# Optimization experiments

Hardware: AMD Instinct MI355X
Metric: run time of the kernel (lower is better)

Reference implementation:

```python
import jax, jax.numpy as jnp
import numpy as np

B, C, H, W = 32, 512, 32, 32
TXT_DIM, M, NUM_HEADS = 768, 77, 8
HEAD_DIM = C // NUM_HEADS
SCALE = HEAD_DIM ** -0.5


def setup_inputs() -> dict:
    key = jax.random.key(0)
    ks = jax.random.split(key, 9)
    x = jax.random.normal(ks[0], (B, C, H, W), dtype=jnp.float32)
    text_emb = jax.random.normal(ks[1], (B, M, TXT_DIM), dtype=jnp.float32)
    attention_mask = jnp.ones((B, M), dtype=jnp.int32)
    # Linear params (PyTorch convention: weight [out, in], bias [out])
    s_q = 1.0 / np.sqrt(C)
    s_kv = 1.0 / np.sqrt(TXT_DIM)
    Wq = jax.random.uniform(ks[2], (C, C), jnp.float32, -s_q, s_q)
    bq = jax.random.uniform(ks[3], (C,), jnp.float32, -s_q, s_q)
    Wk = jax.random.uniform(ks[4], (C, TXT_DIM), jnp.float32, -s_kv, s_kv)
    bk = jax.random.uniform(ks[5], (C,), jnp.float32, -s_kv, s_kv)
    Wv = jax.random.uniform(ks[6], (C, TXT_DIM), jnp.float32, -s_kv, s_kv)
    bv = jax.random.uniform(ks[7], (C,), jnp.float32, -s_kv, s_kv)
    return {"x": x, "text_emb": text_emb, "attention_mask": attention_mask,
            "Wq": Wq, "bq": bq, "Wk": Wk, "bk": bk, "Wv": Wv, "bv": bv}


def reference(x, text_emb, attention_mask, Wq, bq, Wk, bk, Wv, bv):
    b, c, h, w = x.shape
    n = h * w
    x_flat = x.reshape(b, c, n).transpose(0, 2, 1)          # [B, N, C]
    Q = x_flat @ Wq.T + bq                                   # [B, N, C]
    K = text_emb @ Wk.T + bk                                 # [B, M, C]
    V = text_emb @ Wv.T + bv                                 # [B, M, C]
    Q = Q.reshape(b, n, NUM_HEADS, HEAD_DIM)
    K = K.reshape(b, -1, NUM_HEADS, HEAD_DIM)
    V = V.reshape(b, -1, NUM_HEADS, HEAD_DIM)
    # scores: [B, heads, N, M]
    scores = jnp.einsum('bnhd,bmhd->bhnm', Q, K) * SCALE
    mask = attention_mask[:, None, None, :] != 0
    scores = jnp.where(mask, scores, -jnp.inf)
    probs = jax.nn.softmax(scores, axis=-1)
    out = jnp.einsum('bhnm,bmhd->bnhd', probs, V)            # [B, N, heads, d]
    out = out.reshape(b, n, c).transpose(0, 2, 1).reshape(b, c, h, w)
    return out
```

## Files before the change

kernel.cpp:

```cpp
#include <hip/hip_runtime.h>
#include <math.h>

#define BB   32
#define CC   512
#define HWN  1024
#define MM   77
#define TXT  768
#define NH   8
#define HD   64
#define SCALEF 0.125f
#define MPAD 96
#define KVROWS (BB*MPAD)
#define AP   40
#define PP   104
#define OSP  132

typedef __attribute__((ext_vector_type(8))) short          bf16x8;
typedef __attribute__((ext_vector_type(8))) unsigned short us8;
typedef __attribute__((ext_vector_type(4))) float          f32x4;

__device__ inline unsigned short f2bf(float f) {
    union { float f; unsigned u; } v; v.f = f;
    unsigned r = v.u + 0x7fff + ((v.u >> 16) & 1);
    return (unsigned short)(r >> 16);
}

__device__ inline void gload_lds16(const void* g, void* l) {
    __builtin_amdgcn_global_load_lds(
        (const __attribute__((address_space(1))) void*)g,
        (__attribute__((address_space(3))) void*)l, 16, 0, 0);
}

__global__ __launch_bounds__(256) void wcvt_kernel(
    const float* __restrict__ src, unsigned short* __restrict__ dst)
{
    const int i = blockIdx.x * 256 + threadIdx.x;
    const float4 v = ((const float4*)src)[i];
    ushort4 o;
    o.x = f2bf(v.x); o.y = f2bf(v.y); o.z = f2bf(v.z); o.w = f2bf(v.w);
    ((ushort4*)dst)[i] = o;
}

__global__ __launch_bounds__(256) void tcvt_kernel(
    const float* __restrict__ x, unsigned short* __restrict__ xT)
{
    const int nt = blockIdx.x, ct = blockIdx.y, b = blockIdx.z;
    const int n0 = nt * 64, c0 = ct * 64;
    __shared__ float tile[64][65];
    const int t = threadIdx.x;
    const float* xb = x + (size_t)b * CC * HWN;
    {
        const int c = t >> 2;
        #pragma unroll
        for (int j = 0; j < 4; ++j) {
            const int f4 = (t & 3) + j * 4;
            const float4 v = *(const float4*)&xb[(size_t)(c0 + c) * HWN + n0 + f4 * 4];
            tile[c][f4 * 4 + 0] = v.x; tile[c][f4 * 4 + 1] = v.y;
            tile[c][f4 * 4 + 2] = v.z; tile[c][f4 * 4 + 3] = v.w;
        }
    }
    __syncthreads();
    unsigned short* xTb = xT + (size_t)b * HWN * CC;
    #pragma unroll
    for (int j = 0; j < 2; ++j) {
        const int n = (t >> 3) + j * 32;
        const int c8 = (t & 7) * 8;
        us8 o;
        #pragma unroll
        for (int i = 0; i < 8; ++i) o[i] = f2bf(tile[c8 + i][n]);
        *(us8*)&xTb[(size_t)(n0 + n) * CC + c0 + c8] = o;
    }
}

__global__ __launch_bounds__(256) void qgemm_mfma(
    const unsigned short* __restrict__ xT, const unsigned short* __restrict__ Wqb,
    const float* __restrict__ bq, unsigned short* __restrict__ Qb)
{
    const int rt = blockIdx.x, ct = blockIdx.y;
    const int row0 = rt * 128, co0 = ct * 128;
    __shared__ unsigned short As[128 * 32];
    __shared__ unsigned short Bs[128 * 32];
    const int t = threadIdx.x;
    const int lane = t & 63, w = t >> 6;
    const int wr = w >> 1, wc = w & 1;
    const int lm = lane & 15, quad = lane >> 4;
    const int lrow = lane >> 2, lk = (lane & 3) * 8;

    f32x4 acc[4][4] = {};

    for (int k0 = 0; k0 < CC; k0 += 32) {
        #pragma unroll
        for (int p = 0; p < 2; ++p) {
            const int chunk = w * 2 + p;
            gload_lds16(&xT[(size_t)(row0 + chunk * 16 + lrow) * CC + k0 + lk],
                        &As[chunk * 512]);
            gload_lds16(&Wqb[(size_t)(co0 + chunk * 16 + lrow) * CC + k0 + lk],
                        &Bs[chunk * 512]);
        }
        __syncthreads();
        bf16x8 a[4], bfr[4];
        #pragma unroll
        for (int i = 0; i < 4; ++i)
            a[i] = *(const bf16x8*)&As[(wr * 64 + i * 16 + lm) * 32 + quad * 8];
        #pragma unroll
        for (int i = 0; i < 4; ++i)
            bfr[i] = *(const bf16x8*)&Bs[(wc * 64 + i * 16 + lm) * 32 + quad * 8];
        #pragma unroll
        for (int mi = 0; mi < 4; ++mi)
            #pragma unroll
            for (int ni = 0; ni < 4; ++ni)
                acc[mi][ni] = __builtin_amdgcn_mfma_f32_16x16x32_bf16(
                    a[mi], bfr[ni], acc[mi][ni], 0, 0, 0);
        __syncthreads();
    }

    #pragma unroll
    for (int ni = 0; ni < 4; ++ni) {
        const int col = co0 + wc * 64 + ni * 16 + lm;
        const float bias = bq[col];
        #pragma unroll
        for (int mi = 0; mi < 4; ++mi) {
            #pragma unroll
            for (int j = 0; j < 4; ++j) {
                const int row = row0 + wr * 64 + mi * 16 + quad * 4 + j;
                Qb[(size_t)row * CC + col] = f2bf(acc[mi][ni][j] + bias);
            }
        }
    }
}

__global__ __launch_bounds__(256) void kvgemm_mfma(
    const float* __restrict__ te,
    const float* __restrict__ Wk, const float* __restrict__ bk,
    const float* __restrict__ Wv, const float* __restrict__ bv,
    unsigned short* __restrict__ Kb, unsigned short* __restrict__ Vt)
{
    const int rt = blockIdx.x, ctc = blockIdx.y;
    const int row0 = rt * 64;
    const int isV = (ctc >= 8);
    const float* W = isV ? Wv : Wk;
    const float* bias_p = isV ? bv : bk;
    const int co0 = (ctc & 7) * 64;

    __shared__ unsigned short As[64 * AP];
    __shared__ unsigned short Bs[64 * AP];
    const int t = threadIdx.x;
    const int lane = t & 63, w = t >> 6;
    const int wr = w >> 1, wc = w & 1;
    const int lm = lane & 15, quad = lane >> 4;
    const int chunk = t & 3, srow = t >> 2;

    f32x4 acc[2][2] = {};

    const int rflat = row0 + srow;
    const int b_i = rflat / MPAD, m_i = rflat % MPAD;
    const float* terow = te + ((size_t)b_i * MM + min(m_i, MM - 1)) * TXT;
    const float* wrow  = W + (size_t)(co0 + srow) * TXT;

    for (int k0 = 0; k0 < TXT; k0 += 32) {
        {
            const float4 f0 = *(const float4*)&terow[k0 + chunk * 8];
            const float4 f1 = *(const float4*)&terow[k0 + chunk * 8 + 4];
            us8 o;
            o[0] = f2bf(f0.x); o[1] = f2bf(f0.y); o[2] = f2bf(f0.z); o[3] = f2bf(f0.w);
            o[4] = f2bf(f1.x); o[5] = f2bf(f1.y); o[6] = f2bf(f1.z); o[7] = f2bf(f1.w);
            *(us8*)&As[srow * AP + chunk * 8] = o;

            const float4 g0 = *(const float4*)&wrow[k0 + chunk * 8];
            const float4 g1 = *(const float4*)&wrow[k0 + chunk * 8 + 4];
            us8 ob;
            ob[0] = f2bf(g0.x); ob[1] = f2bf(g0.y); ob[2] = f2bf(g0.z); ob[3] = f2bf(g0.w);
            ob[4] = f2bf(g1.x); ob[5] = f2bf(g1.y); ob[6] = f2bf(g1.z); ob[7] = f2bf(g1.w);
            *(us8*)&Bs[srow * AP + chunk * 8] = ob;
        }
        __syncthreads();
        bf16x8 a[2], bfr[2];
        #pragma unroll
        for (int i = 0; i < 2; ++i)
            a[i] = *(const bf16x8*)&As[(wr * 32 + i * 16 + lm) * AP + quad * 8];
        #pragma unroll
        for (int i = 0; i < 2; ++i)
            bfr[i] = *(const bf16x8*)&Bs[(wc * 32 + i * 16 + lm) * AP + quad * 8];
        #pragma unroll
        for (int mi = 0; mi < 2; ++mi)
            #pragma unroll
            for (int ni = 0; ni < 2; ++ni)
                acc[mi][ni] = __builtin_amdgcn_mfma_f32_16x16x32_bf16(
                    a[mi], bfr[ni], acc[mi][ni], 0, 0, 0);
        __syncthreads();
    }

    #pragma unroll
    for (int ni = 0; ni < 2; ++ni) {
        const int col = co0 + wc * 32 + ni * 16 + lm;
        const float bias = bias_p[col];
        #pragma unroll
        for (int mi = 0; mi < 2; ++mi) {
            #pragma unroll
            for (int j = 0; j < 2 * 2; ++j) {
                const int row = row0 + wr * 32 + mi * 16 + quad * 4 + j;
                const int bo = row / MPAD, mo = row % MPAD;
                const unsigned short hv = f2bf(acc[mi][ni][j] + bias);
                if (isV) {
                    Vt[((size_t)bo * CC + col) * MPAD + mo] = hv;
                } else if (mo < MM) {
                    Kb[((size_t)bo * MM + mo) * CC + col] = hv;
                }
            }
        }
    }
}

__global__ __launch_bounds__(256) void attn_mfma(
    const unsigned short* __restrict__ Qb, const unsigned short* __restrict__ Kb,
    const unsigned short* __restrict__ Vt, const int* __restrict__ amask,
    float* __restrict__ out)
{
    const int ntile = blockIdx.x;
    const int h     = blockIdx.y;
    const int b     = blockIdx.z;
    const int row0  = ntile * 128;

    __shared__ char smem[64 * OSP * 4];
    __shared__ float msk[80];
    unsigned short* Ps = (unsigned short*)smem;
    float* Os = (float*)smem;

    const int t = threadIdx.x;
    const int w = t >> 6, lane = t & 63;
    const int lm = lane & 15, quad = lane >> 4;

    {
        const int r = t >> 1, off = 80 + (t & 1) * 8;
        us8 z = {0, 0, 0, 0, 0, 0, 0, 0};
        *(us8*)&Ps[r * PP + off] = z;
    }
    if (t < 80) msk[t] = (t < MM && amask[b * MM + t] != 0) ? 0.f : -INFINITY;
    __syncthreads();

    f32x4 s[2][5] = {};
    const unsigned short* qbase = Qb + ((size_t)b * HWN + row0) * CC + h * HD;
    const unsigned short* kbase = Kb + (size_t)b * MM * CC + h * HD;
    #pragma unroll
    for (int ks = 0; ks < 2; ++ks) {
        bf16x8 a[2], kf[5];
        #pragma unroll
        for (int mt = 0; mt < 2; ++mt)
            a[mt] = *(const bf16x8*)&qbase[(size_t)((w * 2 + mt) * 16 + lm) * CC + ks * 32 + quad * 8];
        #pragma unroll
        for (int n = 0; n < 5; ++n) {
            const int kr = min(n * 16 + lm, MM - 1);
            kf[n] = *(const bf16x8*)&kbase[(size_t)kr * CC + ks * 32 + quad * 8];
        }
        #pragma unroll
        for (int mt = 0; mt < 2; ++mt)
            #pragma unroll
            for (int n = 0; n < 5; ++n)
                s[mt][n] = __builtin_amdgcn_mfma_f32_16x16x32_bf16(a[mt], kf[n], s[mt][n], 0, 0, 0);
    }

    float inv[2][4];
    #pragma unroll
    for (int mt = 0; mt < 2; ++mt) {
        #pragma unroll
        for (int j = 0; j < 4; ++j) {
            float v[5];
            #pragma unroll
            for (int n = 0; n < 5; ++n)
                v[n] = s[mt][n][j] * SCALEF + msk[n * 16 + lm];
            float mx = fmaxf(fmaxf(fmaxf(v[0], v[1]), fmaxf(v[2], v[3])), v[4]);
            mx = fmaxf(mx, __shfl_xor(mx, 1, 64));
            mx = fmaxf(mx, __shfl_xor(mx, 2, 64));
            mx = fmaxf(mx, __shfl_xor(mx, 4, 64));
            mx = fmaxf(mx, __shfl_xor(mx, 8, 64));
            float sum = 0.f;
            #pragma unroll
            for (int n = 0; n < 5; ++n) { v[n] = __expf(v[n] - mx); sum += v[n]; }
            sum += __shfl_xor(sum, 1, 64);
            sum += __shfl_xor(sum, 2, 64);
            sum += __shfl_xor(sum, 4, 64);
            sum += __shfl_xor(sum, 8, 64);
            inv[mt][j] = 1.0f / sum;
            const int mrow = (w * 2 + mt) * 16 + quad * 4 + j;
            #pragma unroll
            for (int n = 0; n < 5; ++n)
                Ps[mrow * PP + n * 16 + lm] = f2bf(v[n]);
        }
    }
    __syncthreads();

    f32x4 o[2][4] = {};
    const unsigned short* vbase = Vt + ((size_t)b * CC + h * HD) * MPAD;
    #pragma unroll
    for (int ks = 0; ks < 3; ++ks) {
        bf16x8 a[2], vf[4];
        #pragma unroll
        for (int mt = 0; mt < 2; ++mt)
            a[mt] = *(const bf16x8*)&Ps[((w * 2 + mt) * 16 + lm) * PP + ks * 32 + quad * 8];
        #pragma unroll
        for (int n = 0; n < 4; ++n)
            vf[n] = *(const bf16x8*)&vbase[(size_t)(n * 16 + lm) * MPAD + ks * 32 + quad * 8];
        #pragma unroll
        for (int mt = 0; mt < 2; ++mt)
            #pragma unroll
            for (int n = 0; n < 4; ++n)
                o[mt][n] = __builtin_amdgcn_mfma_f32_16x16x32_bf16(a[mt], vf[n], o[mt][n], 0, 0, 0);
    }
    __syncthreads();

    #pragma unroll
    for (int mt = 0; mt < 2; ++mt) {
        #pragma unroll
        for (int n = 0; n < 4; ++n) {
            const int col = n * 16 + lm;
            const int r0 = (w * 2 + mt) * 16 + quad * 4;
            float4 st;
            st.x = o[mt][n][0] * inv[mt][0];
            st.y = o[mt][n][1] * inv[mt][1];
            st.z = o[mt][n][2] * inv[mt][2];
            st.w = o[mt][n][3] * inv[mt][3];
            *(float4*)&Os[col * OSP + r0] = st;
        }
    }
    __syncthreads();

    float* obase = out + ((size_t)b * CC + h * HD) * HWN + row0;
    #pragma unroll
    for (int p = 0; p < 8; ++p) {
        const int idx = p * 256 + t;
        const int col = idx >> 5;
        const int r4  = idx & 31;
        const float4 v = *(const float4*)&Os[col * OSP + r4 * 4];
        *(float4*)&obase[(size_t)col * HWN + r4 * 4] = v;
    }
}

extern "C" void kernel_launch(void* const* d_in, const int* in_sizes, int n_in,
                              void* d_out, int out_size, void* d_ws, size_t ws_size,
                              hipStream_t stream)
{
    const float* x     = (const float*)d_in[0];
    const float* te    = (const float*)d_in[1];
    const int*   amask = (const int*)d_in[2];
    const float* Wq    = (const float*)d_in[3];
    const float* bq    = (const float*)d_in[4];
    const float* Wk    = (const float*)d_in[5];
    const float* bk    = (const float*)d_in[6];
    const float* Wv    = (const float*)d_in[7];
    const float* bv    = (const float*)d_in[8];
    float* out = (float*)d_out;

    unsigned short* xT  = (unsigned short*)d_ws;
    unsigned short* Qb  = xT + (size_t)BB * HWN * CC;
    unsigned short* Kb  = Qb + (size_t)BB * HWN * CC;
    unsigned short* Vt  = Kb + (size_t)BB * MM * CC;
    unsigned short* Wqb = Vt + (size_t)BB * CC * MPAD;

    wcvt_kernel<<<dim3(CC * CC / 4 / 256), 256, 0, stream>>>(Wq, Wqb);
    tcvt_kernel<<<dim3(16, 8, BB), 256, 0, stream>>>(x, xT);
    qgemm_mfma<<<dim3(256, 4), 256, 0, stream>>>(xT, Wqb, bq, Qb);
    kvgemm_mfma<<<dim3(KVROWS / 64, 16), 256, 0, stream>>>(te, Wk, bk, Wv, bv, Kb, Vt);
    attn_mfma<<<dim3(8, NH, BB), 256, 0, stream>>>(Qb, Kb, Vt, amask, out);
}
```

Baseline: 233.2 us.

## Merge conversion kernels and fuse Q/K/V GEMMs into one launch

Combines the weight conversion and the x transpose-convert into a single prep kernel that also pre-converts Wk, Wv and text_emb to bf16. The Q GEMM and the K/V GEMM become one kernel with a shared 128x128 tile path that loads directly into LDS, replacing the old K/V kernel's small 64x64 tiles with in-loop fp32->bf16 conversion. This cuts launches from five to three and lets the K/V work overlap with the Q GEMM tail, at the cost of extra workspace and a divergent prologue/epilogue.

```diff
diff --git a/kernel.cpp b/kernel.cpp
--- a/kernel.cpp
+++ b/kernel.cpp
@@ -11,7 +11,6 @@
 #define SCALEF 0.125f
 #define MPAD 96
 #define KVROWS (BB*MPAD)
-#define AP   40
 #define PP   104
 #define OSP  132
 
@@ -31,53 +30,73 @@
         (__attribute__((address_space(3))) void*)l, 16, 0, 0);
 }
 
-__global__ __launch_bounds__(256) void wcvt_kernel(
-    const float* __restrict__ src, unsigned short* __restrict__ dst)
+#define TGRID 4096
+#define CV_WQ 65536
+#define CV_WK 98304
+#define CV_WV 98304
+#define CV_TE 473088
+#define CVTOT (CV_WQ + CV_WK + CV_WV + CV_TE)
+
+__global__ __launch_bounds__(256) void prep_kernel(
+    const float* __restrict__ x, const float* __restrict__ te,
+    const float* __restrict__ Wq, const float* __restrict__ Wk,
+    const float* __restrict__ Wv,
+    unsigned short* __restrict__ xT, unsigned short* __restrict__ teb,
+    unsigned short* __restrict__ Wqb, unsigned short* __restrict__ Wkb,
+    unsigned short* __restrict__ Wvb)
 {
-    const int i = blockIdx.x * 256 + threadIdx.x;
-    const float4 v = ((const float4*)src)[i];
-    ushort4 o;
-    o.x = f2bf(v.x); o.y = f2bf(v.y); o.z = f2bf(v.z); o.w = f2bf(v.w);
-    ((ushort4*)dst)[i] = o;
-}
-
-__global__ __launch_bounds__(256) void tcvt_kernel(
-    const float* __restrict__ x, unsigned short* __restrict__ xT)
+    const int bid = blockIdx.x;
+    const int t = threadIdx.x;
+
+    if (bid < TGRID) {
+        const int nt = bid & 15, ct = (bid >> 4) & 7, b = bid >> 7;
+        const int n0 = nt * 64, c0 = ct * 64;
+        __shared__ float tile[64][65];
+        const float* xb = x + (size_t)b * CC * HWN;
+        {
+            const int c = t >> 2;
+            #pragma unroll
+            for (int j = 0; j < 4; ++j) {
+                const int f4 = (t & 3) + j * 4;
+                const float4 v = *(const float4*)&xb[(size_t)(c0 + c) * HWN + n0 + f4 * 4];
+                tile[c][f4 * 4 + 0] = v.x; tile[c][f4 * 4 + 1] = v.y;
+                tile[c][f4 * 4 + 2] = v.z; tile[c][f4 * 4 + 3] = v.w;
+            }
+        }
+        __syncthreads();
+        unsigned short* xTb = xT + (size_t)b * HWN * CC;
+        #pragma unroll
+        for (int j = 0; j < 2; ++j) {
+            const int n = (t >> 3) + j * 32;
+            const int c8 = (t & 7) * 8;
+            us8 o;
+            #pragma unroll
+            for (int i = 0; i < 8; ++i) o[i] = f2bf(tile[c8 + i][n]);
+            *(us8*)&xTb[(size_t)(n0 + n) * CC + c0 + c8] = o;
+        }
+    } else {
+        const int idx = (bid - TGRID) * 256 + t;
+        const float* src; unsigned short* dst; int off;
+        if (idx < CV_WQ)                    { src = Wq; dst = Wqb; off = idx; }
+        else if (idx < CV_WQ + CV_WK)       { src = Wk; dst = Wkb; off = idx - CV_WQ; }
+        else if (idx < CV_WQ + CV_WK + CV_WV) { src = Wv; dst = Wvb; off = idx - CV_WQ - CV_WK; }
+        else                                { src = te; dst = teb; off = idx - CV_WQ - CV_WK - CV_WV; }
+        const float4 v = ((const float4*)src)[off];
+        ushort4 o;
+        o.x = f2bf(v.x); o.y = f2bf(v.y); o.z = f2bf(v.z); o.w = f2bf(v.w);
+        ((ushort4*)dst)[off] = o;
+    }
+}
+
+__global__ __launch_bounds__(256) void gemm_all(
+    const unsigned short* __restrict__ xT, const unsigned short* __restrict__ Wqb,
+    const float* __restrict__ bq, unsigned short* __restrict__ Qb,
+    const unsigned short* __restrict__ teb,
+    const unsigned short* __restrict__ Wkb, const float* __restrict__ bk,
+    const unsigned short* __restrict__ Wvb, const float* __restrict__ bv,
+    unsigned short* __restrict__ Kb, unsigned short* __restrict__ Vt)
 {
-    const int nt = blockIdx.x, ct = blockIdx.y, b = blockIdx.z;
-    const int n0 = nt * 64, c0 = ct * 64;
-    __shared__ float tile[64][65];
-    const int t = threadIdx.x;
-    const float* xb = x + (size_t)b * CC * HWN;
-    {
-        const int c = t >> 2;
-        #pragma unroll
-        for (int j = 0; j < 4; ++j) {
-            const int f4 = (t & 3) + j * 4;
-            const float4 v = *(const float4*)&xb[(size_t)(c0 + c) * HWN + n0 + f4 * 4];
-            tile[c][f4 * 4 + 0] = v.x; tile[c][f4 * 4 + 1] = v.y;
-            tile[c][f4 * 4 + 2] = v.z; tile[c][f4 * 4 + 3] = v.w;
-        }
-    }
-    __syncthreads();
-    unsigned short* xTb = xT + (size_t)b * HWN * CC;
-    #pragma unroll
-    for (int j = 0; j < 2; ++j) {
-        const int n = (t >> 3) + j * 32;
-        const int c8 = (t & 7) * 8;
-        us8 o;
-        #pragma unroll
-        for (int i = 0; i < 8; ++i) o[i] = f2bf(tile[c8 + i][n]);
-        *(us8*)&xTb[(size_t)(n0 + n) * CC + c0 + c8] = o;
-    }
-}
-
-__global__ __launch_bounds__(256) void qgemm_mfma(
-    const unsigned short* __restrict__ xT, const unsigned short* __restrict__ Wqb,
-    const float* __restrict__ bq, unsigned short* __restrict__ Qb)
-{
-    const int rt = blockIdx.x, ct = blockIdx.y;
-    const int row0 = rt * 128, co0 = ct * 128;
+    const int bid = blockIdx.x;
     __shared__ unsigned short As[128 * 32];
     __shared__ unsigned short Bs[128 * 32];
     const int t = threadIdx.x;
@@ -86,17 +105,43 @@
     const int lm = lane & 15, quad = lane >> 4;
     const int lrow = lane >> 2, lk = (lane & 3) * 8;
 
+    const unsigned short *gA0, *gA1, *gB0, *gB1;
+    int kIters, mode, row0, co0;
+
+    if (bid < 1024) {
+        mode = 0;
+        const int rt = bid & 255, ct = bid >> 8;
+        row0 = rt * 128; co0 = ct * 128;
+        kIters = CC / 32;
+        gA0 = xT  + (size_t)(row0 + (w * 2 + 0) * 16 + lrow) * CC + lk;
+        gA1 = xT  + (size_t)(row0 + (w * 2 + 1) * 16 + lrow) * CC + lk;
+        gB0 = Wqb + (size_t)(co0 + (w * 2 + 0) * 16 + lrow) * CC + lk;
+        gB1 = Wqb + (size_t)(co0 + (w * 2 + 1) * 16 + lrow) * CC + lk;
+    } else {
+        const int id = bid - 1024;
+        const int rt = id % 24, cc = id / 24;
+        const int isV = (cc >= 4);
+        mode = isV ? 2 : 1;
+        row0 = rt * 128; co0 = (cc & 3) * 128;
+        kIters = TXT / 32;
+        const unsigned short* Wb = isV ? Wvb : Wkb;
+        const int rp0 = row0 + (w * 2 + 0) * 16 + lrow;
+        const int rp1 = row0 + (w * 2 + 1) * 16 + lrow;
+        const int b0i = rp0 / MPAD, m0i = min(rp0 % MPAD, MM - 1);
+        const int b1i = rp1 / MPAD, m1i = min(rp1 % MPAD, MM - 1);
+        gA0 = teb + (size_t)(b0i * MM + m0i) * TXT + lk;
+        gA1 = teb + (size_t)(b1i * MM + m1i) * TXT + lk;
+        gB0 = Wb + (size_t)(co0 + (w * 2 + 0) * 16 + lrow) * TXT + lk;
+        gB1 = Wb + (size_t)(co0 + (w * 2 + 1) * 16 + lrow) * TXT + lk;
+    }
+
     f32x4 acc[4][4] = {};
 
-    for (int k0 = 0; k0 < CC; k0 += 32) {
-        #pragma unroll
-        for (int p = 0; p < 2; ++p) {
-            const int chunk = w * 2 + p;
-            gload_lds16(&xT[(size_t)(row0 + chunk * 16 + lrow) * CC + k0 + lk],
-                        &As[chunk * 512]);
-            gload_lds16(&Wqb[(size_t)(co0 + chunk * 16 + lrow) * CC + k0 + lk],
-                        &Bs[chunk * 512]);
-        }
+    for (int k = 0; k < kIters; ++k) {
+        gload_lds16(gA0 + k * 32, &As[(w * 2 + 0) * 512]);
+        gload_lds16(gA1 + k * 32, &As[(w * 2 + 1) * 512]);
+        gload_lds16(gB0 + k * 32, &Bs[(w * 2 + 0) * 512]);
+        gload_lds16(gB1 + k * 32, &Bs[(w * 2 + 1) * 512]);
         __syncthreads();
         bf16x8 a[4], bfr[4];
         #pragma unroll
@@ -114,97 +159,38 @@
         __syncthreads();
     }
 
-    #pragma unroll
-    for (int ni = 0; ni < 4; ++ni) {
-        const int col = co0 + wc * 64 + ni * 16 + lm;
-        const float bias = bq[col];
-        #pragma unroll
-        for (int mi = 0; mi < 4; ++mi) {
-            #pragma unroll
-            for (int j = 0; j < 4; ++j) {
-                const int row = row0 + wr * 64 + mi * 16 + quad * 4 + j;
-                Qb[(size_t)row * CC + col] = f2bf(acc[mi][ni][j] + bias);
+    if (mode == 0) {
+        #pragma unroll
+        for (int ni = 0; ni < 4; ++ni) {
+            const int col = co0 + wc * 64 + ni * 16 + lm;
+            const float bias = bq[col];
+            #pragma unroll
+            for (int mi = 0; mi < 4; ++mi) {
+                #pragma unroll
+                for (int j = 0; j < 4; ++j) {
+                    const int row = row0 + wr * 64 + mi * 16 + quad * 4 + j;
+                    Qb[(size_t)row * CC + col] = f2bf(acc[mi][ni][j] + bias);
+                }
             }
         }
-    }
-}
-
-__global__ __launch_bounds__(256) void kvgemm_mfma(
-    const float* __restrict__ te,
-    const float* __restrict__ Wk, const float* __restrict__ bk,
-    const float* __restrict__ Wv, const float* __restrict__ bv,
-    unsigned short* __restrict__ Kb, unsigned short* __restrict__ Vt)
-{
-    const int rt = blockIdx.x, ctc = blockIdx.y;
-    const int row0 = rt * 64;
-    const int isV = (ctc >= 8);
-    const float* W = isV ? Wv : Wk;
-    const float* bias_p = isV ? bv : bk;
-    const int co0 = (ctc & 7) * 64;
-
-    __shared__ unsigned short As[64 * AP];
-    __shared__ unsigned short Bs[64 * AP];
-    const int t = threadIdx.x;
-    const int lane = t & 63, w = t >> 6;
-    const int wr = w >> 1, wc = w & 1;
-    const int lm = lane & 15, quad = lane >> 4;
-    const int chunk = t & 3, srow = t >> 2;
-
-    f32x4 acc[2][2] = {};
-
-    const int rflat = row0 + srow;
-    const int b_i = rflat / MPAD, m_i = rflat % MPAD;
-    const float* terow = te + ((size_t)b_i * MM + min(m_i, MM - 1)) * TXT;
-    const float* wrow  = W + (size_t)(co0 + srow) * TXT;
-
-    for (int k0 = 0; k0 < TXT; k0 += 32) {
-        {
-            const float4 f0 = *(const float4*)&terow[k0 + chunk * 8];
-            const float4 f1 = *(const float4*)&terow[k0 + chunk * 8 + 4];
-            us8 o;
-            o[0] = f2bf(f0.x); o[1] = f2bf(f0.y); o[2] = f2bf(f0.z); o[3] = f2bf(f0.w);
-            o[4] = f2bf(f1.x); o[5] = f2bf(f1.y); o[6] = f2bf(f1.z); o[7] = f2bf(f1.w);
-            *(us8*)&As[srow * AP + chunk * 8] = o;
-
-            const float4 g0 = *(const float4*)&wrow[k0 + chunk * 8];
-            const float4 g1 = *(const float4*)&wrow[k0 + chunk * 8 + 4];
-            us8 ob;
-            ob[0] = f2bf(g0.x); ob[1] = f2bf(g0.y); ob[2] = f2bf(g0.z); ob[3] = f2bf(g0.w);
-            ob[4] = f2bf(g1.x); ob[5] = f2bf(g1.y); ob[6] = f2bf(g1.z); ob[7] = f2bf(g1.w);
-            *(us8*)&Bs[srow * AP + chunk * 8] = ob;
-        }
-        __syncthreads();
-        bf16x8 a[2], bfr[2];
-        #pragma unroll
-        for (int i = 0; i < 2; ++i)
-            a[i] = *(const bf16x8*)&As[(wr * 32 + i * 16 + lm) * AP + quad * 8];
-        #pragma unroll
-        for (int i = 0; i < 2; ++i)
-            bfr[i] = *(const bf16x8*)&Bs[(wc * 32 + i * 16 + lm) * AP + quad * 8];
-        #pragma unroll
-        for (int mi = 0; mi < 2; ++mi)
-            #pragma unroll
-            for (int ni = 0; ni < 2; ++ni)
-                acc[mi][ni] = __builtin_amdgcn_mfma_f32_16x16x32_bf16(
-                    a[mi], bfr[ni], acc[mi][ni], 0, 0, 0);
-        __syncthreads();
-    }
-
-    #pragma unroll
-    for (int ni = 0; ni < 2; ++ni) {
-        const int col = co0 + wc * 32 + ni * 16 + lm;
-        const float bias = bias_p[col];
-        #pragma unroll
-        for (int mi = 0; mi < 2; ++mi) {
-            #pragma unroll
-            for (int j = 0; j < 2 * 2; ++j) {
-                const int row = row0 + wr * 32 + mi * 16 + quad * 4 + j;
-                const int bo = row / MPAD, mo = row % MPAD;
-                const unsigned short hv = f2bf(acc[mi][ni][j] + bias);
-                if (isV) {
-                    Vt[((size_t)bo * CC + col) * MPAD + mo] = hv;
-                } else if (mo < MM) {
-                    Kb[((size_t)bo * MM + mo) * CC + col] = hv;
+    } else {
+        const float* bias_p = (mode == 2) ? bv : bk;
+        #pragma unroll
+        for (int ni = 0; ni < 4; ++ni) {
+            const int col = co0 + wc * 64 + ni * 16 + lm;
+            const float bias = bias_p[col];
+            #pragma unroll
+            for (int mi = 0; mi < 4; ++mi) {
+                #pragma unroll
+                for (int j = 0; j < 4; ++j) {
+                    const int row = row0 + wr * 64 + mi * 16 + quad * 4 + j;
+                    const int bo = row / MPAD, mo = row % MPAD;
+                    const unsigned short hv = f2bf(acc[mi][ni][j] + bias);
+                    if (mode == 2) {
+                        Vt[((size_t)bo * CC + col) * MPAD + mo] = hv;
+                    } else if (mo < MM) {
+                        Kb[((size_t)bo * MM + mo) * CC + col] = hv;
+                    }
                 }
             }
         }
@@ -351,14 +337,17 @@
     float* out = (float*)d_out;
 
     unsigned short* xT  = (unsigned short*)d_ws;
-    unsigned short* Qb  = xT + (size_t)BB * HWN * CC;
-    unsigned short* Kb  = Qb + (size_t)BB * HWN * CC;
-    unsigned short* Vt  = Kb + (size_t)BB * MM * CC;
-    unsigned short* Wqb = Vt + (size_t)BB * CC * MPAD;
-
-    wcvt_kernel<<<dim3(CC * CC / 4 / 256), 256, 0, stream>>>(Wq, Wqb);
-    tcvt_kernel<<<dim3(16, 8, BB), 256, 0, stream>>>(x, xT);
-    qgemm_mfma<<<dim3(256, 4), 256, 0, stream>>>(xT, Wqb, bq, Qb);
-    kvgemm_mfma<<<dim3(KVROWS / 64, 16), 256, 0, stream>>>(te, Wk, bk, Wv, bv, Kb, Vt);
+    unsigned short* Qb  = xT  + (size_t)BB * HWN * CC;
+    unsigned short* Kb  = Qb  + (size_t)BB * HWN * CC;
+    unsigned short* Vt  = Kb  + (size_t)BB * MM * CC;
+    unsigned short* Wqb = Vt  + (size_t)BB * CC * MPAD;
+    unsigned short* Wkb = Wqb + (size_t)CC * CC;
+    unsigned short* Wvb = Wkb + (size_t)CC * TXT;
+    unsigned short* teb = Wvb + (size_t)CC * TXT;
+
+    prep_kernel<<<dim3(TGRID + CVTOT / 256), 256, 0, stream>>>(
+        x, te, Wq, Wk, Wv, xT, teb, Wqb, Wkb, Wvb);
+    gemm_all<<<dim3(1024 + 192), 256, 0, stream>>>(
+        xT, Wqb, bq, Qb, teb, Wkb, bk, Wvb, bv, Kb, Vt);
     attn_mfma<<<dim3(8, NH, BB), 256, 0, stream>>>(Qb, Kb, Vt, amask, out);
 }
```

New measurement: 223.8 us. 1.04x faster.
